# Optimization experiments

Measured on AMD Instinct MI355X. Metric: run time of the kernel, lower is better.

The kernel has to match this reference:

```python
import jax, jax.numpy as jnp
import numpy as np

P_FACTOR = 3.0
EPS = 1e-12  # F.normalize eps


def _l2norm(x):
    n = jnp.sqrt(jnp.sum(x * x, axis=-1, keepdims=True))
    return x / jnp.maximum(n, EPS)


def setup_inputs() -> dict:
    key = jax.random.key(0)
    ks = jax.random.split(key, 7)
    B, N, F, E = 4096, 16384, 768, 512
    X = jax.random.normal(ks[0], (B, F), dtype=jnp.float32)
    D = jax.random.normal(ks[1], (N, F), dtype=jnp.float32)
    r = jax.random.uniform(ks[2], (N, 1), dtype=jnp.float32)
    g_w = jax.random.normal(ks[3], (E, F), dtype=jnp.float32) * (1.0 / np.sqrt(F))
    g_b = jax.random.normal(ks[4], (E,), dtype=jnp.float32) * 0.01
    h_w = jax.random.normal(ks[5], (1, 1), dtype=jnp.float32)
    h_b = jax.random.normal(ks[6], (1,), dtype=jnp.float32) * 0.01
    return {"X": X, "D": D, "r": r, "g_w": g_w, "g_b": g_b, "h_w": h_w, "h_b": h_b}


def reference(X, D, r, g_w, g_b, h_w, h_b):
    # r in {0..1} -> {-1..1}
    r2 = r * 2.0 - 1.0
    # feature embedding g applied to both queries and exemplars
    Xe = X @ g_w.T + g_b            # [B, E]
    De = D @ g_w.T + g_b            # [N, E]
    # cosine similarity
    a = _l2norm(Xe) @ _l2norm(De).T  # [B, N]
    # power-law sign activation: |a|^p * sign(a)
    a = jnp.power(jnp.abs(a), P_FACTOR) * jnp.sign(a)
    # weighted exemplar sum (echo)
    echo = a @ r2                    # [B, 1]
    # class embedding h (Linear 1 -> 1)
    logits = echo @ h_w.T + h_b      # [B, 1]
    preds = jax.nn.sigmoid(logits)
    return (logits, preds)
```

## Files before the change

### kernel.cpp

```cpp
#include <hip/hip_runtime.h>
#include <hip/hip_bf16.h>
#include <hip/hip_fp8.h>
#include <stdint.h>

#define P_B 4096
#define P_N 16384
#define P_F 768
#define P_E 512
#define NKT_F 24
#define NKTP_E 8
#define CPAD 776
#define EPAD3 520

typedef __attribute__((ext_vector_type(8))) __bf16 bf16x8;
typedef __attribute__((ext_vector_type(4))) float f32x4;

__device__ __forceinline__ unsigned short bfbits(float x) {
    __bf16 h = (__bf16)x;
    union { __bf16 h; unsigned short u; } cv;
    cv.h = h;
    return cv.u;
}
__device__ __forceinline__ float bf2f(unsigned short u) {
    union { float f; unsigned int i; } cv;
    cv.i = ((unsigned int)u) << 16;
    return cv.f;
}
__device__ __forceinline__ unsigned char f8bits(float x) {
    __hip_fp8_e4m3 h(x);
    return (unsigned char)h.__x;
}


__global__ __launch_bounds__(256) void convert_pack_kernel(
    const float* __restrict__ gw, unsigned short* __restrict__ gwpk,
    float* __restrict__ zbase)
{
    __shared__ unsigned short T[16 * CPAD];
    const int tid = threadIdx.x;
    const int rb = blockIdx.x;

    const int z = rb * 256 + tid;
    if (z < P_B + P_N + P_B) zbase[z] = 0.0f;
    if (rb >= 32) return;

    const float* src = gw + (size_t)rb * 16 * P_F;
    unsigned short* dstbase = gwpk + (size_t)rb * NKT_F * 512;

#pragma unroll
    for (int it = 0; it < 12; ++it) {
        const int flat = it * 1024 + tid * 4;
        const int row = flat / P_F;
        const int col = flat - row * P_F;
        const float4 v = *(const float4*)(src + (size_t)row * P_F + col);
        unsigned short* t = &T[row * CPAD + col];
        t[0] = bfbits(v.x); t[1] = bfbits(v.y); t[2] = bfbits(v.z); t[3] = bfbits(v.w);
    }
    __syncthreads();

#pragma unroll
    for (int it = 0; it < 6; ++it) {
        const int m = it * 256 + tid;
        const int kt = m >> 6;
        const int lane = m & 63;
        const int r = lane & 15;
        const int k = kt * 32 + (lane >> 4) * 8;
        const uint4 frag = *(const uint4*)(&T[r * CPAD + k]);
        *(uint4*)(dstbase + (size_t)(kt * 64 + lane) * 8) = frag;
    }
}

__global__ __launch_bounds__(256, 2) void embed_pk_kernel(
    const float* __restrict__ X, const float* __restrict__ D,
    const unsigned short* __restrict__ gwpk, const float* __restrict__ gb,
    unsigned char* __restrict__ embpk8, float* __restrict__ norm2)
{
    __shared__ union {
        unsigned short T[32 * CPAD];
        unsigned short Es[32 * EPAD3];
    } sh;
    const int tid = threadIdx.x, lane = tid & 63, wave = tid >> 6;
    const int q = lane >> 4, c = lane & 15;
    const int rowTile = blockIdx.x;
    const float* src = (rowTile < 128) ? (X + (size_t)rowTile * 32 * P_F)
                                       : (D + (size_t)(rowTile - 128) * 32 * P_F);

#pragma unroll
    for (int it = 0; it < 24; ++it) {
        const int flat = it * 1024 + tid * 4;
        const int row = flat / P_F;
        const int col = flat - row * P_F;
        const float4 v = *(const float4*)(src + (size_t)row * P_F + col);
        unsigned short* t = &sh.T[row * CPAD + col];
        t[0] = bfbits(v.x); t[1] = bfbits(v.y); t[2] = bfbits(v.z); t[3] = bfbits(v.w);
    }
    __syncthreads();

    const unsigned short* pb[8];
#pragma unroll
    for (int j = 0; j < 8; j++)
        pb[j] = gwpk + ((size_t)(wave * 8 + j) * NKT_F * 64 + lane) * 8;

    f32x4 acc[2][8];
    const f32x4 zero = {0.f, 0.f, 0.f, 0.f};
#pragma unroll
    for (int i = 0; i < 2; i++)
#pragma unroll
        for (int j = 0; j < 8; j++) acc[i][j] = zero;

#pragma unroll
    for (int kt = 0; kt < NKT_F; ++kt) {
        bf16x8 af[2], bfr[8];
#pragma unroll
        for (int i = 0; i < 2; i++)
            af[i] = *(const bf16x8*)(&sh.T[(i * 16 + (lane & 15)) * CPAD
                                           + kt * 32 + (lane >> 4) * 8]);
#pragma unroll
        for (int j = 0; j < 8; j++) bfr[j] = *(const bf16x8*)(pb[j] + (size_t)kt * 512);
        __builtin_amdgcn_s_setprio(1);
#pragma unroll
        for (int i = 0; i < 2; i++)
#pragma unroll
            for (int j = 0; j < 8; j++)
                acc[i][j] = __builtin_amdgcn_mfma_f32_16x16x32_bf16(af[i], bfr[j], acc[i][j], 0, 0, 0);
        __builtin_amdgcn_s_setprio(0);
    }
    __syncthreads();

    float ss[2][4];
#pragma unroll
    for (int i = 0; i < 2; i++)
#pragma unroll
        for (int r = 0; r < 4; r++) ss[i][r] = 0.f;
#pragma unroll
    for (int j = 0; j < 8; j++) {
        const int lc = wave * 128 + j * 16 + c;
        const float bias = gb[lc];
#pragma unroll
        for (int i = 0; i < 2; i++) {
#pragma unroll
            for (int r = 0; r < 4; r++) {
                const int lr = i * 16 + q * 4 + r;
                const float v = acc[i][j][r] + bias;
                const unsigned short hb = bfbits(v);
                sh.Es[lr * EPAD3 + lc] = hb;
                const float vs = bf2f(hb);
                ss[i][r] = fmaf(vs, vs, ss[i][r]);
            }
        }
    }
#pragma unroll
    for (int i = 0; i < 2; i++)
#pragma unroll
        for (int r = 0; r < 4; r++) {
            float s = ss[i][r];
            s += __shfl_xor(s, 1);
            s += __shfl_xor(s, 2);
            s += __shfl_xor(s, 4);
            s += __shfl_xor(s, 8);
            ss[i][r] = s;
        }
    if (c == 0) {
#pragma unroll
        for (int i = 0; i < 2; i++)
#pragma unroll
            for (int r = 0; r < 4; r++) {
                const int rowg = rowTile * 32 + i * 16 + q * 4 + r;
                atomicAdd(&norm2[rowg], ss[i][r]);
            }
    }
    __syncthreads();

#pragma unroll
    for (int it = 0; it < 4; ++it) {
        const int m = it * 256 + tid;
        const int rbl = m >> 9;
        const int rest = m & 511;
        const int ktpl = rest >> 6;
        const int lane2 = rest & 63;
        const int r2 = lane2 & 15;
        const int q2 = lane2 >> 4;
        const int lr = rbl * 16 + r2;
        const unsigned short* e0 = &sh.Es[lr * EPAD3 + ktpl * 64 + q2 * 8];
        const unsigned short* e1 = e0 + 32;
        union { unsigned char b[16]; uint4 v; } outw;
#pragma unroll
        for (int t = 0; t < 8; t++) outw.b[t]     = f8bits(bf2f(e0[t]));
#pragma unroll
        for (int t = 0; t < 8; t++) outw.b[8 + t] = f8bits(bf2f(e1[t]));
        const size_t rb = (size_t)(rowTile * 2 + rbl);
        *(uint4*)(embpk8 + ((rb * NKTP_E + (size_t)ktpl) * 64 + lane2) * 16) = outw.v;
    }
}

__global__ void finalize_kernel(float* __restrict__ nf, const float* __restrict__ r)
{
    const int i = blockIdx.x * 256 + threadIdx.x;
    if (i >= P_B + P_N) return;
    float nrm = sqrtf(nf[i]);
    nrm = fmaxf(nrm, 1e-12f);
    const float inv = 1.0f / nrm;
    float w = inv * inv * inv;
    if (i >= P_B) {
        const float rv = r[i - P_B];
        w *= (2.0f * rv - 1.0f);
    }
    nf[i] = w;
}

__global__ __launch_bounds__(256, 2) void echo_pk_kernel(
    const unsigned char* __restrict__ embpk8, const float* __restrict__ fbuf,
    float* __restrict__ echo)
{
    const int tid = threadIdx.x, lane = tid & 63, wave = tid >> 6;
    const int q = lane >> 4, c = lane & 15;
    const int bid = blockIdx.x;
    const int sb = bid >> 6, w = bid & 63;
    const int btile = (sb & 3) * 8 + (w & 7);
    const int ntile = (sb >> 2) * 8 + (w >> 3);
    const int row0 = btile * 128;
    const int col0 = ntile * 128;
    const int rbA0 = btile * 8 + (wave >> 1) * 4;
    const int rbB0 = 256 + ntile * 8 + (wave & 1) * 4;

    const unsigned char* pa[4];
    const unsigned char* pb[4];
#pragma unroll
    for (int i = 0; i < 4; i++)
        pa[i] = embpk8 + ((size_t)(rbA0 + i) * NKTP_E * 64 + lane) * 16;
#pragma unroll
    for (int j = 0; j < 4; j++)
        pb[j] = embpk8 + ((size_t)(rbB0 + j) * NKTP_E * 64 + lane) * 16;

    f32x4 acc[4][4];
    const f32x4 zero = {0.f, 0.f, 0.f, 0.f};
#pragma unroll
    for (int i = 0; i < 4; i++)
#pragma unroll
        for (int j = 0; j < 4; j++) acc[i][j] = zero;

#pragma unroll
    for (int ktp = 0; ktp < NKTP_E; ++ktp) {
        union { uint4 v; long l[2]; } ua[4], ub[4];
#pragma unroll
        for (int i = 0; i < 4; i++) ua[i].v = *(const uint4*)(pa[i] + (size_t)ktp * 1024);
#pragma unroll
        for (int j = 0; j < 4; j++) ub[j].v = *(const uint4*)(pb[j] + (size_t)ktp * 1024);
        __builtin_amdgcn_s_setprio(1);
#pragma unroll
        for (int h = 0; h < 2; h++)
#pragma unroll
            for (int i = 0; i < 4; i++)
#pragma unroll
                for (int j = 0; j < 4; j++)
                    acc[i][j] = __builtin_amdgcn_mfma_f32_16x16x32_fp8_fp8(
                        ua[i].l[h], ub[j].l[h], acc[i][j], 0, 0, 0);
        __builtin_amdgcn_s_setprio(0);
    }

    const float* fX = fbuf;
    const float* fD = fbuf + P_B;
    float wc[4];
#pragma unroll
    for (int j = 0; j < 4; j++) wc[j] = fD[col0 + (wave & 1) * 64 + j * 16 + c];
    float p[4][4];
#pragma unroll
    for (int i = 0; i < 4; i++)
#pragma unroll
        for (int r = 0; r < 4; r++) p[i][r] = 0.f;
#pragma unroll
    for (int i = 0; i < 4; i++)
#pragma unroll
        for (int j = 0; j < 4; j++)
#pragma unroll
            for (int r = 0; r < 4; r++) {
                const float v = acc[i][j][r];
                const float v3 = v * v * v;
                p[i][r] = fmaf(v3, wc[j], p[i][r]);
            }
#pragma unroll
    for (int i = 0; i < 4; i++)
#pragma unroll
        for (int r = 0; r < 4; r++) {
            float s = p[i][r];
            s += __shfl_xor(s, 1);
            s += __shfl_xor(s, 2);
            s += __shfl_xor(s, 4);
            s += __shfl_xor(s, 8);
            p[i][r] = s;
        }
    if (c == 0) {
#pragma unroll
        for (int i = 0; i < 4; i++)
#pragma unroll
            for (int r = 0; r < 4; r++) {
                const int rowg = row0 + (wave >> 1) * 64 + i * 16 + q * 4 + r;
                atomicAdd(&echo[rowg], p[i][r] * fX[rowg]);
            }
    }
}

__global__ void head_kernel(const float* __restrict__ echo, const float* __restrict__ hw,
                            const float* __restrict__ hb, float* __restrict__ out)
{
    const int i = blockIdx.x * 256 + threadIdx.x;
    if (i >= P_B) return;
    const float logit = fmaf(echo[i], hw[0], hb[0]);
    out[i] = logit;
    out[P_B + i] = 1.0f / (1.0f + expf(-logit));
}

extern "C" void kernel_launch(void* const* d_in, const int* in_sizes, int n_in,
                              void* d_out, int out_size, void* d_ws, size_t ws_size,
                              hipStream_t stream)
{
    const float* X  = (const float*)d_in[0];
    const float* D  = (const float*)d_in[1];
    const float* r  = (const float*)d_in[2];
    const float* gw = (const float*)d_in[3];
    const float* gb = (const float*)d_in[4];
    const float* hw = (const float*)d_in[5];
    const float* hb = (const float*)d_in[6];
    float* out = (float*)d_out;

    char* ws = (char*)d_ws;
    const size_t gwpk_bytes   = (size_t)32 * NKT_F * 64 * 8 * 2;
    const size_t embpk8_bytes = (size_t)1280 * NKTP_E * 64 * 16;

    unsigned short* gwpk   = (unsigned short*)ws;
    unsigned char*  embpk8 = (unsigned char*)(ws + gwpk_bytes);
    float* norm2 = (float*)(ws + gwpk_bytes + embpk8_bytes);
    float* echo = norm2 + (P_B + P_N);

    convert_pack_kernel<<<dim3(97), 256, 0, stream>>>(gw, gwpk, norm2);
    embed_pk_kernel<<<dim3(640), 256, 0, stream>>>(X, D, gwpk, gb, embpk8, norm2);
    finalize_kernel<<<dim3((P_B + P_N + 255) / 256), 256, 0, stream>>>(norm2, r);
    echo_pk_kernel<<<dim3(4096), 256, 0, stream>>>(embpk8, norm2, echo);
    head_kernel<<<dim3((P_B + 255) / 256), 256, 0, stream>>>(echo, hw, hb, out);
}
```

Measured before the change: 181.6 us.

## Pipeline input tile staging with MFMA compute in embedding kernel

Splits the 768-column input tile load into three 256-column phases. The next phase's global loads are held in registers while the current phase's MFMAs run, then written to shared memory behind a barrier. This hides global load latency behind compute instead of loading the whole tile up front. The launch bound also rises to 3 blocks per SM, which limits registers and risks spills given the 8 float4 staging registers plus 64 accumulator values per thread.

```diff
diff --git a/kernel.cpp b/kernel.cpp
--- a/kernel.cpp
+++ b/kernel.cpp
@@ -70,7 +70,7 @@
     }
 }
 
-__global__ __launch_bounds__(256, 2) void embed_pk_kernel(
+__global__ __launch_bounds__(256, 3) void embed_pk_kernel(
     const float* __restrict__ X, const float* __restrict__ D,
     const unsigned short* __restrict__ gwpk, const float* __restrict__ gb,
     unsigned char* __restrict__ embpk8, float* __restrict__ norm2)
@@ -85,14 +85,18 @@
     const float* src = (rowTile < 128) ? (X + (size_t)rowTile * 32 * P_F)
                                        : (D + (size_t)(rowTile - 128) * 32 * P_F);
 
-#pragma unroll
-    for (int it = 0; it < 24; ++it) {
-        const int flat = it * 1024 + tid * 4;
-        const int row = flat / P_F;
-        const int col = flat - row * P_F;
-        const float4 v = *(const float4*)(src + (size_t)row * P_F + col);
-        unsigned short* t = &sh.T[row * CPAD + col];
-        t[0] = bfbits(v.x); t[1] = bfbits(v.y); t[2] = bfbits(v.z); t[3] = bfbits(v.w);
+    const int srow = wave;
+    const int scol = (tid & 63) * 4;
+
+    float4 sv[8];
+#pragma unroll
+    for (int it = 0; it < 8; ++it)
+        sv[it] = *(const float4*)(src + (size_t)(it * 4 + srow) * P_F + scol);
+#pragma unroll
+    for (int it = 0; it < 8; ++it) {
+        unsigned short* t = &sh.T[(it * 4 + srow) * CPAD + scol];
+        t[0] = bfbits(sv[it].x); t[1] = bfbits(sv[it].y);
+        t[2] = bfbits(sv[it].z); t[3] = bfbits(sv[it].w);
     }
     __syncthreads();
 
@@ -109,21 +113,41 @@
         for (int j = 0; j < 8; j++) acc[i][j] = zero;
 
 #pragma unroll
-    for (int kt = 0; kt < NKT_F; ++kt) {
-        bf16x8 af[2], bfr[8];
-#pragma unroll
-        for (int i = 0; i < 2; i++)
-            af[i] = *(const bf16x8*)(&sh.T[(i * 16 + (lane & 15)) * CPAD
-                                           + kt * 32 + (lane >> 4) * 8]);
-#pragma unroll
-        for (int j = 0; j < 8; j++) bfr[j] = *(const bf16x8*)(pb[j] + (size_t)kt * 512);
-        __builtin_amdgcn_s_setprio(1);
-#pragma unroll
-        for (int i = 0; i < 2; i++)
-#pragma unroll
-            for (int j = 0; j < 8; j++)
-                acc[i][j] = __builtin_amdgcn_mfma_f32_16x16x32_bf16(af[i], bfr[j], acc[i][j], 0, 0, 0);
-        __builtin_amdgcn_s_setprio(0);
+    for (int phase = 0; phase < 3; ++phase) {
+        if (phase < 2) {
+            const int cc = (phase + 1) * 256;
+#pragma unroll
+            for (int it = 0; it < 8; ++it)
+                sv[it] = *(const float4*)(src + (size_t)(it * 4 + srow) * P_F + cc + scol);
+        }
+#pragma unroll
+        for (int kk = 0; kk < 8; ++kk) {
+            const int kt = phase * 8 + kk;
+            bf16x8 af[2], bfr[8];
+#pragma unroll
+            for (int i = 0; i < 2; i++)
+                af[i] = *(const bf16x8*)(&sh.T[(i * 16 + (lane & 15)) * CPAD
+                                               + kt * 32 + (lane >> 4) * 8]);
+#pragma unroll
+            for (int j = 0; j < 8; j++) bfr[j] = *(const bf16x8*)(pb[j] + (size_t)kt * 512);
+            __builtin_amdgcn_s_setprio(1);
+#pragma unroll
+            for (int i = 0; i < 2; i++)
+#pragma unroll
+                for (int j = 0; j < 8; j++)
+                    acc[i][j] = __builtin_amdgcn_mfma_f32_16x16x32_bf16(af[i], bfr[j], acc[i][j], 0, 0, 0);
+            __builtin_amdgcn_s_setprio(0);
+        }
+        if (phase < 2) {
+            const int cc = (phase + 1) * 256;
+#pragma unroll
+            for (int it = 0; it < 8; ++it) {
+                unsigned short* t = &sh.T[(it * 4 + srow) * CPAD + cc + scol];
+                t[0] = bfbits(sv[it].x); t[1] = bfbits(sv[it].y);
+                t[2] = bfbits(sv[it].z); t[3] = bfbits(sv[it].w);
+            }
+            __syncthreads();
+        }
     }
     __syncthreads();
 
```

After: 207.7 us. 1.14x slower.

## Fold norm finalization into echo kernel and drop zero-init atomics

Applied to the files above, without the earlier changes.

Removes finalize_kernel by computing the inverse-cube norm weights inline in the echo kernel's epilogue, with the r-based sign weights folded in there. The embed kernel now reduces per-row squared norms across waves in shared memory and writes them directly instead of using atomics, so the norm buffer no longer needs zero-initialisation. Echo zeroing moves into the embed kernel. This saves one kernel launch and some global atomics, but each echo block recomputes sqrt and reciprocal for its columns and rows.

```diff
diff --git a/kernel.cpp b/kernel.cpp
--- a/kernel.cpp
+++ b/kernel.cpp
@@ -33,16 +33,11 @@
 
 
 __global__ __launch_bounds__(256) void convert_pack_kernel(
-    const float* __restrict__ gw, unsigned short* __restrict__ gwpk,
-    float* __restrict__ zbase)
+    const float* __restrict__ gw, unsigned short* __restrict__ gwpk)
 {
     __shared__ unsigned short T[16 * CPAD];
     const int tid = threadIdx.x;
     const int rb = blockIdx.x;
-
-    const int z = rb * 256 + tid;
-    if (z < P_B + P_N + P_B) zbase[z] = 0.0f;
-    if (rb >= 32) return;
 
     const float* src = gw + (size_t)rb * 16 * P_F;
     unsigned short* dstbase = gwpk + (size_t)rb * NKT_F * 512;
@@ -73,17 +68,23 @@
 __global__ __launch_bounds__(256, 2) void embed_pk_kernel(
     const float* __restrict__ X, const float* __restrict__ D,
     const unsigned short* __restrict__ gwpk, const float* __restrict__ gb,
-    unsigned char* __restrict__ embpk8, float* __restrict__ norm2)
+    unsigned char* __restrict__ embpk8, float* __restrict__ norm2,
+    float* __restrict__ echo)
 {
     __shared__ union {
         unsigned short T[32 * CPAD];
-        unsigned short Es[32 * EPAD3];
+        struct {
+            unsigned short Es[32 * EPAD3];
+            float R[4][32];
+        } e;
     } sh;
     const int tid = threadIdx.x, lane = tid & 63, wave = tid >> 6;
     const int q = lane >> 4, c = lane & 15;
     const int rowTile = blockIdx.x;
     const float* src = (rowTile < 128) ? (X + (size_t)rowTile * 32 * P_F)
                                        : (D + (size_t)(rowTile - 128) * 32 * P_F);
+
+    if (rowTile < 16) echo[rowTile * 256 + tid] = 0.0f;
 
 #pragma unroll
     for (int it = 0; it < 24; ++it) {
@@ -143,7 +144,7 @@
                 const int lr = i * 16 + q * 4 + r;
                 const float v = acc[i][j][r] + bias;
                 const unsigned short hb = bfbits(v);
-                sh.Es[lr * EPAD3 + lc] = hb;
+                sh.e.Es[lr * EPAD3 + lc] = hb;
                 const float vs = bf2f(hb);
                 ss[i][r] = fmaf(vs, vs, ss[i][r]);
             }
@@ -164,12 +165,15 @@
 #pragma unroll
         for (int i = 0; i < 2; i++)
 #pragma unroll
-            for (int r = 0; r < 4; r++) {
-                const int rowg = rowTile * 32 + i * 16 + q * 4 + r;
-                atomicAdd(&norm2[rowg], ss[i][r]);
-            }
+            for (int r = 0; r < 4; r++)
+                sh.e.R[wave][i * 16 + q * 4 + r] = ss[i][r];
     }
     __syncthreads();
+
+    if (tid < 32) {
+        const float s = sh.e.R[0][tid] + sh.e.R[1][tid] + sh.e.R[2][tid] + sh.e.R[3][tid];
+        norm2[rowTile * 32 + tid] = s;
+    }
 
 #pragma unroll
     for (int it = 0; it < 4; ++it) {
@@ -181,7 +185,7 @@
         const int r2 = lane2 & 15;
         const int q2 = lane2 >> 4;
         const int lr = rbl * 16 + r2;
-        const unsigned short* e0 = &sh.Es[lr * EPAD3 + ktpl * 64 + q2 * 8];
+        const unsigned short* e0 = &sh.e.Es[lr * EPAD3 + ktpl * 64 + q2 * 8];
         const unsigned short* e1 = e0 + 32;
         union { unsigned char b[16]; uint4 v; } outw;
 #pragma unroll
@@ -193,24 +197,9 @@
     }
 }
 
-__global__ void finalize_kernel(float* __restrict__ nf, const float* __restrict__ r)
-{
-    const int i = blockIdx.x * 256 + threadIdx.x;
-    if (i >= P_B + P_N) return;
-    float nrm = sqrtf(nf[i]);
-    nrm = fmaxf(nrm, 1e-12f);
-    const float inv = 1.0f / nrm;
-    float w = inv * inv * inv;
-    if (i >= P_B) {
-        const float rv = r[i - P_B];
-        w *= (2.0f * rv - 1.0f);
-    }
-    nf[i] = w;
-}
-
 __global__ __launch_bounds__(256, 2) void echo_pk_kernel(
-    const unsigned char* __restrict__ embpk8, const float* __restrict__ fbuf,
-    float* __restrict__ echo)
+    const unsigned char* __restrict__ embpk8, const float* __restrict__ norm2,
+    const float* __restrict__ rr, float* __restrict__ echo)
 {
     const int tid = threadIdx.x, lane = tid & 63, wave = tid >> 6;
     const int q = lane >> 4, c = lane & 15;
@@ -258,11 +247,15 @@
         __builtin_amdgcn_s_setprio(0);
     }
 
-    const float* fX = fbuf;
-    const float* fD = fbuf + P_B;
     float wc[4];
 #pragma unroll
-    for (int j = 0; j < 4; j++) wc[j] = fD[col0 + (wave & 1) * 64 + j * 16 + c];
+    for (int j = 0; j < 4; j++) {
+        const int cd = col0 + (wave & 1) * 64 + j * 16 + c;
+        const float nD = norm2[P_B + cd];
+        const float nrmD = fmaxf(sqrtf(nD), 1e-12f);
+        const float invD = 1.0f / nrmD;
+        wc[j] = invD * invD * invD * (2.0f * rr[cd] - 1.0f);
+    }
     float p[4][4];
 #pragma unroll
     for (int i = 0; i < 4; i++)
@@ -295,7 +288,10 @@
 #pragma unroll
             for (int r = 0; r < 4; r++) {
                 const int rowg = row0 + (wave >> 1) * 64 + i * 16 + q * 4 + r;
-                atomicAdd(&echo[rowg], p[i][r] * fX[rowg]);
+                const float nX = norm2[rowg];
+                const float nrmX = fmaxf(sqrtf(nX), 1e-12f);
+                const float invX = 1.0f / nrmX;
+                atomicAdd(&echo[rowg], p[i][r] * (invX * invX * invX));
             }
     }
 }
@@ -332,9 +328,8 @@
     float* norm2 = (float*)(ws + gwpk_bytes + embpk8_bytes);
     float* echo = norm2 + (P_B + P_N);
 
-    convert_pack_kernel<<<dim3(97), 256, 0, stream>>>(gw, gwpk, norm2);
-    embed_pk_kernel<<<dim3(640), 256, 0, stream>>>(X, D, gwpk, gb, embpk8, norm2);
-    finalize_kernel<<<dim3((P_B + P_N + 255) / 256), 256, 0, stream>>>(norm2, r);
-    echo_pk_kernel<<<dim3(4096), 256, 0, stream>>>(embpk8, norm2, echo);
+    convert_pack_kernel<<<dim3(32), 256, 0, stream>>>(gw, gwpk);
+    embed_pk_kernel<<<dim3(640), 256, 0, stream>>>(X, D, gwpk, gb, embpk8, norm2, echo);
+    echo_pk_kernel<<<dim3(4096), 256, 0, stream>>>(embpk8, norm2, r, echo);
     head_kernel<<<dim3((P_B + 255) / 256), 256, 0, stream>>>(echo, hw, hb, out);
 }
```

After: 184.3 us. Within noise of the previous version (+1.4%).
